# Kernel optimization log

Measured on AMD Instinct MI355X. Metric: run time of the kernel, lower is better.

The kernel has to match this reference:

```python
import jax, jax.numpy as jnp
import numpy as np

D_IN, D, N, L, NW, NC, NH, DC = 1536, 256, 16, 2, 64, 234, 4, 4
B_SZ, T_LEN = 256, 64
N_SITES, N_HOURS, META = 20, 24, 16


def setup_inputs() -> dict:
    key = jax.random.key(0)
    ks = iter(jax.random.split(key, 64))
    def rn(shape, scale=0.02):
        return jax.random.normal(next(ks), shape, jnp.float32) * scale
    inp = {}
    inp["emb"] = jax.random.normal(next(ks), (B_SZ, T_LEN, D_IN), jnp.float32)
    inp["perch_logits"] = jax.random.normal(next(ks), (B_SZ, T_LEN, NC), jnp.float32)
    inp["site_ids"] = jax.random.randint(next(ks), (B_SZ,), 0, N_SITES)
    inp["hours"] = jax.random.randint(next(ks), (B_SZ,), 0, N_HOURS)
    # input_proj: Linear(d_input, d_model) + LayerNorm
    inp["in_w"] = rn((D, D_IN)); inp["in_b"] = jnp.zeros((D,))
    inp["ln0_g"] = jnp.ones((D,)); inp["ln0_b"] = jnp.zeros((D,))
    inp["pos_enc"] = rn((1, NW, D))
    inp["site_emb"] = rn((N_SITES, META), 1.0)
    inp["hour_emb"] = rn((N_HOURS, META), 1.0)
    inp["meta_w"] = rn((D, 2 * META)); inp["meta_b"] = jnp.zeros((D,))
    # SelectiveSSM params, stacked [L, 2(dir)] over layers and fwd/bwd directions
    inp["ssm_in_w"] = rn((L, 2, 2 * D, D))
    inp["ssm_conv_w"] = rn((L, 2, D, DC), 0.1)
    inp["ssm_conv_b"] = jnp.zeros((L, 2, D))
    inp["ssm_dt_w"] = rn((L, 2, D, D)); inp["ssm_dt_b"] = jnp.zeros((L, 2, D))
    A = jnp.arange(1, N + 1, dtype=jnp.float32)
    inp["ssm_A_log"] = jnp.log(jnp.broadcast_to(A, (L, 2, D, N)))
    inp["ssm_Dp"] = jnp.ones((L, 2, D))
    inp["ssm_B_w"] = rn((L, 2, N, D)); inp["ssm_C_w"] = rn((L, 2, N, D))
    inp["merge_w"] = rn((L, D, 2 * D)); inp["merge_b"] = jnp.zeros((L, D))
    inp["ln_g"] = jnp.ones((L, D)); inp["ln_b"] = jnp.zeros((L, D))
    # TemporalCrossAttention
    inp["qkv_w"] = rn((3 * D, D)); inp["qkv_b"] = jnp.zeros((3 * D,))
    inp["ao_w"] = rn((D, D)); inp["ao_b"] = jnp.zeros((D,))
    inp["ca_ln1_g"] = jnp.ones((D,)); inp["ca_ln1_b"] = jnp.zeros((D,))
    inp["ffn_w1"] = rn((2 * D, D)); inp["ffn_b1"] = jnp.zeros((2 * D,))
    inp["ffn_w2"] = rn((D, 2 * D)); inp["ffn_b2"] = jnp.zeros((D,))
    inp["ca_ln2_g"] = jnp.ones((D,)); inp["ca_ln2_b"] = jnp.zeros((D,))
    # prototype head
    inp["prototypes"] = rn((NC, D))
    inp["proto_temp"] = jnp.asarray(5.0, jnp.float32)
    inp["class_bias"] = jnp.zeros((NC,))
    inp["fusion_alpha"] = jnp.zeros((NC,))
    return inp


def _ln(x, g, b, eps=1e-5):
    m = x.mean(-1, keepdims=True)
    v = ((x - m) ** 2).mean(-1, keepdims=True)
    return (x - m) * jax.lax.rsqrt(v + eps) * g + b


def _l2norm(x):
    n = jnp.sqrt((x * x).sum(-1, keepdims=True))
    return x / jnp.maximum(n, 1e-12)


def _ssm(x, in_w, conv_w, conv_b, dt_w, dt_b, A_log, Dp, B_w, C_w):
    """SelectiveSSM.forward. x: [B,T,D]. (z gate / out_proj unused in original.)"""
    Bb, T, Dd = x.shape
    x_ssm = (x @ in_w.T)[..., :Dd]  # first chunk of in_proj output
    # depthwise causal conv (Conv1d pad=DC-1 then slice [:T] == left pad)
    xp = jnp.pad(x_ssm, ((0, 0), (DC - 1, 0), (0, 0)))
    xc = sum(xp[:, k:k + T, :] * conv_w[:, k] for k in range(DC)) + conv_b
    xc = jax.nn.silu(xc)
    dt = jax.nn.softplus(xc @ dt_w.T + dt_b)       # [B,T,D]
    A = -jnp.exp(A_log)                            # [D,N]
    Bm = xc @ B_w.T                                # [B,T,N]
    Cm = xc @ C_w.T                                # [B,T,N]

    def step(h, inp):
        dt_t, B_t, C_t, x_t = inp                  # [B,D],[B,N],[B,N],[B,D]
        dA = jnp.exp(A * dt_t[..., None])          # [B,D,N]
        h = h * dA + (x_t * dt_t)[..., None] * B_t[:, None, :]
        y = jnp.einsum('bdn,bn->bd', h, C_t)
        return h, y

    h0 = jnp.zeros((Bb, Dd, A.shape[-1]), x.dtype)
    xs = (dt.transpose(1, 0, 2), Bm.transpose(1, 0, 2),
          Cm.transpose(1, 0, 2), x.transpose(1, 0, 2))
    _, ys = jax.lax.scan(step, h0, xs)             # ys: [T,B,D]
    return ys.transpose(1, 0, 2) + x * Dp


def _mha(x, qkv_w, qkv_b, ao_w, ao_b):
    Bb, T, Dd = x.shape
    dh = Dd // NH
    q, k, v = jnp.split(x @ qkv_w.T + qkv_b, 3, axis=-1)
    rs = lambda t: t.reshape(Bb, T, NH, dh).transpose(0, 2, 1, 3)
    q, k, v = rs(q), rs(k), rs(v)
    att = jax.nn.softmax(jnp.einsum('bhqd,bhkd->bhqk', q, k) / np.sqrt(dh), axis=-1)
    o = jnp.einsum('bhqk,bhkd->bhqd', att, v).transpose(0, 2, 1, 3).reshape(Bb, T, Dd)
    return o @ ao_w.T + ao_b


def reference(emb, perch_logits, site_ids, hours, in_w, in_b, ln0_g, ln0_b,
              pos_enc, site_emb, hour_emb, meta_w, meta_b,
              ssm_in_w, ssm_conv_w, ssm_conv_b, ssm_dt_w, ssm_dt_b,
              ssm_A_log, ssm_Dp, ssm_B_w, ssm_C_w, merge_w, merge_b, ln_g, ln_b,
              qkv_w, qkv_b, ao_w, ao_b, ca_ln1_g, ca_ln1_b,
              ffn_w1, ffn_b1, ffn_w2, ffn_b2, ca_ln2_g, ca_ln2_b,
              prototypes, proto_temp, class_bias, fusion_alpha):
    T = emb.shape[1]
    h = jax.nn.gelu(_ln(emb @ in_w.T + in_b, ln0_g, ln0_b), approximate=False)
    h = h + pos_enc[:, :T, :]
    meta = jnp.concatenate([site_emb[site_ids], hour_emb[hours]], -1) @ meta_w.T + meta_b
    h = h + meta[:, None, :]
    for l in range(L):
        res = h
        hf = _ssm(h, ssm_in_w[l, 0], ssm_conv_w[l, 0], ssm_conv_b[l, 0],
                  ssm_dt_w[l, 0], ssm_dt_b[l, 0], ssm_A_log[l, 0], ssm_Dp[l, 0],
                  ssm_B_w[l, 0], ssm_C_w[l, 0])
        hb = _ssm(h[:, ::-1], ssm_in_w[l, 1], ssm_conv_w[l, 1], ssm_conv_b[l, 1],
                  ssm_dt_w[l, 1], ssm_dt_b[l, 1], ssm_A_log[l, 1], ssm_Dp[l, 1],
                  ssm_B_w[l, 1], ssm_C_w[l, 1])[:, ::-1]
        h = jnp.concatenate([hf, hb], -1) @ merge_w[l].T + merge_b[l]
        h = _ln(h + res, ln_g[l], ln_b[l])
    # TemporalCrossAttention (pre-norm, residual)
    h = h + _mha(_ln(h, ca_ln1_g, ca_ln1_b), qkv_w, qkv_b, ao_w, ao_b)
    x2 = _ln(h, ca_ln2_g, ca_ln2_b)
    h = h + (jax.nn.gelu(x2 @ ffn_w1.T + ffn_b1, approximate=False) @ ffn_w2.T + ffn_b2)
    # prototype similarity head
    sim = (_l2norm(h) @ _l2norm(prototypes).T) * jax.nn.softplus(proto_temp) + class_bias
    alpha = jax.nn.sigmoid(fusion_alpha)
    species_logits = alpha * sim + (1.0 - alpha) * perch_logits
    return species_logits, h
```

## Files before the change

### kernel.cpp

```cpp
#include <hip/hip_runtime.h>
#include <math.h>

typedef float f32x4 __attribute__((ext_vector_type(4)));
typedef short bf16x8 __attribute__((ext_vector_type(8)));

#define DEV static __device__ __forceinline__

constexpr int MROWS = 16384;
constexpr long long MD = 4194304LL;
constexpr long long DTZ = 4718592LL;
constexpr float L2E = 1.44269504088896f;
constexpr float LN2 = 0.69314718055995f;

DEV short f2bf(float f) {
  unsigned u = __float_as_uint(f);
  u += 0x7fffu + ((u >> 16) & 1u);
  return (short)(u >> 16);
}
DEV float wredsum(float v) {
#pragma unroll
  for (int off = 32; off > 0; off >>= 1) v += __shfl_xor(v, off, 64);
  return v;
}
DEV float gelu_f(float x) { return 0.5f * x * (1.f + erff(x * 0.70710678118654752f)); }
DEV float softplus_fast(float x) {
  return (x > 20.f) ? x : log2f(1.f + exp2f(x * L2E)) * LN2;
}
DEV float sigmoid_fast(float x) { return 1.f / (1.f + exp2f(-x * L2E)); }

enum { E_NONE = 0, E_BIAS = 1, E_BIAS_RES = 2, E_GELU_BIAS = 3, E_SIM = 4, E_CONV = 5 };

template <int EPI>
__global__ __launch_bounds__(256) void gemm128(
    const float* __restrict__ A, const float* __restrict__ W, float* __restrict__ C,
    const float* __restrict__ bias, const float* __restrict__ res,
    int K, int ldc,
    long long az, long long wz, long long cz, long long bz,
    const float* __restrict__ xa, const float* __restrict__ xt) {
  constexpr int SBYTES = (EPI == E_CONV) ? 33280 : 27648;
  __shared__ __align__(16) char smem[SBYTES];
  short* As = (short*)smem;
  short* Bs = As + 128 * 72;
  const int z = blockIdx.z;
  A += (long long)z * az;
  W += (long long)z * wz;
  C += (long long)z * cz;
  const float* bi = bias ? bias + (long long)z * bz : bias;
  const int tid = threadIdx.x, lane = tid & 63, wid = tid >> 6;
  const int wm = wid >> 1, wn = wid & 1;
  const int rowBase = blockIdx.y * 128, colBase = blockIdx.x * 64;
  f32x4 acc[4][2];
#pragma unroll
  for (int m = 0; m < 4; ++m)
#pragma unroll
    for (int n = 0; n < 2; ++n) acc[m][n] = f32x4{0.f, 0.f, 0.f, 0.f};
  const int sr = tid >> 3, sc = (tid & 7) << 3;
  f32x4 ra[4][2], rb[2][2];

#define GLOAD(K0)                                                              \
  {                                                                            \
    _Pragma("unroll") for (int p = 0; p < 4; ++p) {                            \
      const float* sa = A + (long long)(rowBase + p * 32 + sr) * K + ((K0) + sc); \
      ra[p][0] = *(const f32x4*)sa;                                            \
      ra[p][1] = *(const f32x4*)(sa + 4);                                      \
    }                                                                          \
    _Pragma("unroll") for (int q = 0; q < 2; ++q) {                            \
      int wr = colBase + q * 32 + sr;                                          \
      wr = (wr < ldc) ? wr : (ldc - 1);                                        \
      const float* sb = W + (long long)wr * K + ((K0) + sc);                   \
      rb[q][0] = *(const f32x4*)sb;                                            \
      rb[q][1] = *(const f32x4*)(sb + 4);                                      \
    }                                                                          \
  }

  GLOAD(0);
  const int nsteps = K >> 6;
  for (int s = 0; s < nsteps; ++s) {
    __syncthreads();
#pragma unroll
    for (int p = 0; p < 4; ++p) {
      bf16x8 pa;
      pa[0] = f2bf(ra[p][0][0]); pa[1] = f2bf(ra[p][0][1]);
      pa[2] = f2bf(ra[p][0][2]); pa[3] = f2bf(ra[p][0][3]);
      pa[4] = f2bf(ra[p][1][0]); pa[5] = f2bf(ra[p][1][1]);
      pa[6] = f2bf(ra[p][1][2]); pa[7] = f2bf(ra[p][1][3]);
      *(bf16x8*)&As[(p * 32 + sr) * 72 + sc] = pa;
    }
#pragma unroll
    for (int q = 0; q < 2; ++q) {
      bf16x8 pb;
      pb[0] = f2bf(rb[q][0][0]); pb[1] = f2bf(rb[q][0][1]);
      pb[2] = f2bf(rb[q][0][2]); pb[3] = f2bf(rb[q][0][3]);
      pb[4] = f2bf(rb[q][1][0]); pb[5] = f2bf(rb[q][1][1]);
      pb[6] = f2bf(rb[q][1][2]); pb[7] = f2bf(rb[q][1][3]);
      *(bf16x8*)&Bs[(q * 32 + sr) * 72 + sc] = pb;
    }
    if (s + 1 < nsteps) GLOAD((s + 1) << 6);
    __syncthreads();
#pragma unroll
    for (int ks = 0; ks < 2; ++ks) {
      const int kb = ks * 32 + (lane >> 4) * 8;
      bf16x8 af[4], bw[2];
#pragma unroll
      for (int m = 0; m < 4; ++m)
        af[m] = *(const bf16x8*)&As[(wm * 64 + m * 16 + (lane & 15)) * 72 + kb];
#pragma unroll
      for (int n = 0; n < 2; ++n)
        bw[n] = *(const bf16x8*)&Bs[(wn * 32 + n * 16 + (lane & 15)) * 72 + kb];
#pragma unroll
      for (int m = 0; m < 4; ++m)
#pragma unroll
        for (int n = 0; n < 2; ++n)
          acc[m][n] = __builtin_amdgcn_mfma_f32_16x16x32_bf16(af[m], bw[n], acc[m][n], 0, 0, 0);
    }
  }
#undef GLOAD

  if constexpr (EPI == E_CONV) {
    float* SX = (float*)smem;
    __syncthreads();
#pragma unroll
    for (int m = 0; m < 4; ++m)
#pragma unroll
      for (int n = 0; n < 2; ++n)
#pragma unroll
        for (int r = 0; r < 4; ++r) {
          const int rl = wm * 64 + m * 16 + ((lane >> 4) << 2) + r;
          const int cl = wn * 32 + n * 16 + (lane & 15);
          SX[rl * 65 + cl] = acc[m][n][r];
        }
    __syncthreads();
    const int c = tid & 63, rg = tid >> 6;
    const int gcol = colBase + c;
    const float* cwp = xa + (long long)z * 1024 + gcol * 4;
    const float wv0 = cwp[0], wv1 = cwp[1], wv2 = cwp[2], wv3 = cwp[3];
    const float cbv = xt[z * 256 + gcol];
#pragma unroll 4
    for (int i = 0; i < 32; ++i) {
      const int lr = rg * 32 + i;
      const int seq = lr >> 6, tau = lr & 63;
      float a = cbv;
#pragma unroll
      for (int k = 0; k < 4; ++k) {
        const int sidx = tau - 3 + k;
        if (sidx >= 0) {
          const int srow = seq * 64 + (z ? 63 - sidx : sidx);
          const float wk = (k == 0) ? wv0 : (k == 1) ? wv1 : (k == 2) ? wv2 : wv3;
          a += SX[srow * 65 + c] * wk;
        }
      }
      a = a * sigmoid_fast(a);
      C[(long long)(rowBase + lr) * ldc + gcol] = a;
    }
    return;
  }

  float sps = 0.f;
  if (EPI == E_SIM) sps = softplus_fast(xt[0]);
#pragma unroll
  for (int m = 0; m < 4; ++m)
#pragma unroll
    for (int n = 0; n < 2; ++n)
#pragma unroll
      for (int r = 0; r < 4; ++r) {
        const int row = rowBase + wm * 64 + m * 16 + ((lane >> 4) << 2) + r;
        const int col = colBase + wn * 32 + n * 16 + (lane & 15);
        if (col < ldc) {
          float v = acc[m][n][r];
          if (EPI == E_BIAS || EPI == E_BIAS_RES || EPI == E_GELU_BIAS) v += bi[col];
          if (EPI == E_BIAS_RES) v += res[(long long)row * ldc + col];
          if (EPI == E_GELU_BIAS) v = gelu_f(v);
          if (EPI == E_SIM) {
            v = v * sps + bi[col];
            const float al = 1.f / (1.f + expf(-xa[col]));
            v = al * v + (1.f - al) * res[(long long)row * ldc + col];
          }
          C[(long long)row * ldc + col] = v;
        }
      }
}

__global__ __launch_bounds__(256) void prep_wcat(
    const float* __restrict__ dt_w, const float* __restrict__ dt_b,
    const float* __restrict__ Bw, const float* __restrict__ Cw,
    float* __restrict__ wcat, float* __restrict__ bcat) {
  const int r = blockIdx.x, ld = blockIdx.y, tid = threadIdx.x;
  float v;
  if (r < 256)      v = dt_w[(long long)ld * 65536 + r * 256 + tid];
  else if (r < 272) v = Bw[(long long)ld * 4096 + (r - 256) * 256 + tid];
  else              v = Cw[(long long)ld * 4096 + (r - 272) * 256 + tid];
  wcat[(long long)ld * 98304 + (long long)r * 256 + tid] = v;
  if (r == 0) bcat[ld * 288 + tid] = dt_b[ld * 256 + tid];
  if (r == 1 && tid < 32) bcat[ld * 288 + 256 + tid] = 0.f;
}

__global__ __launch_bounds__(256) void meta_kernel(
    const int* __restrict__ site_ids, const int* __restrict__ hours,
    const float* __restrict__ site_emb, const float* __restrict__ hour_emb,
    const float* __restrict__ meta_w, const float* __restrict__ meta_b,
    float* __restrict__ out) {
  const int b = blockIdx.x, d = threadIdx.x;
  const int si = site_ids[b], hr = hours[b];
  const float* mw = meta_w + d * 32;
  float acc = meta_b[d];
#pragma unroll
  for (int m = 0; m < 16; ++m) acc += site_emb[si * 16 + m] * mw[m];
#pragma unroll
  for (int m = 0; m < 16; ++m) acc += hour_emb[hr * 16 + m] * mw[16 + m];
  out[b * 256 + d] = acc;
}

template <int MODE>
__global__ __launch_bounds__(256) void ln_kernel(
    const float* __restrict__ in, float* __restrict__ out,
    const float* __restrict__ g, const float* __restrict__ bta,
    const float* __restrict__ pos, const float* __restrict__ mta) {
  const int row = blockIdx.x * 4 + (threadIdx.x >> 6);
  const int lane = threadIdx.x & 63;
  const long long base = (long long)row * 256 + lane * 4;
  f32x4 v = *(const f32x4*)(in + base);
  const float mean = wredsum(v[0] + v[1] + v[2] + v[3]) * (1.f / 256.f);
  f32x4 c = {v[0] - mean, v[1] - mean, v[2] - mean, v[3] - mean};
  const float var = wredsum(c[0] * c[0] + c[1] * c[1] + c[2] * c[2] + c[3] * c[3]) * (1.f / 256.f);
  const float rs = rsqrtf(var + 1e-5f);
  const f32x4 gv = *(const f32x4*)(g + lane * 4);
  const f32x4 bv = *(const f32x4*)(bta + lane * 4);
  f32x4 y;
#pragma unroll
  for (int j = 0; j < 4; ++j) y[j] = c[j] * rs * gv[j] + bv[j];
  if (MODE == 1) {
    const f32x4 pv = *(const f32x4*)(pos + (row & 63) * 256 + lane * 4);
    const f32x4 mv = *(const f32x4*)(mta + (row >> 6) * 256 + lane * 4);
#pragma unroll
    for (int j = 0; j < 4; ++j) y[j] = gelu_f(y[j]) + pv[j] + mv[j];
  }
  *(f32x4*)(out + base) = y;
}

__global__ __launch_bounds__(256) void scan_kernel(
    const float* __restrict__ dtbc, const float* __restrict__ x,
    float* __restrict__ hcat, const float* __restrict__ alog,
    const float* __restrict__ Dpl) {
  __shared__ float bcs[2048];
  const int b = blockIdx.x, dir = blockIdx.y, d = threadIdx.x;
  const float* dz = dtbc + (long long)dir * DTZ;
  for (int idx = d; idx < 2048; idx += 256)
    bcs[idx] = dz[(long long)(b * 64 + (idx >> 5)) * 288 + 256 + (idx & 31)];
  float an2[16];
  const float* al = alog + ((long long)dir * 256 + d) * 16;
#pragma unroll
  for (int n = 0; n < 16; ++n) an2[n] = -expf(al[n]) * L2E;
  const float dp = Dpl[dir * 256 + d];
  float hs[16];
#pragma unroll
  for (int n = 0; n < 16; ++n) hs[n] = 0.f;
  __syncthreads();
  const float* dtr = dz + (long long)b * 64 * 288 + d;
  const float* xr = x + (long long)b * 64 * 256 + d;
  float draw = dtr[0];
  float xv = xr[(dir ? 63 : 0) * 256];
  for (int tau = 0; tau < 64; ++tau) {
    float drawN = 0.f, xvN = 0.f;
    if (tau < 63) {
      drawN = dtr[(tau + 1) * 288];
      xvN = xr[(dir ? (62 - tau) : (tau + 1)) * 256];
    }
    const float dtv = softplus_fast(draw);
    const float u = xv * dtv;
    float y = 0.f;
#pragma unroll
    for (int n = 0; n < 16; ++n) {
      const float dA = exp2f(an2[n] * dtv);
      hs[n] = hs[n] * dA + u * bcs[tau * 32 + n];
      y += hs[n] * bcs[tau * 32 + 16 + n];
    }
    const int to = dir ? 63 - tau : tau;
    hcat[(long long)(b * 64 + to) * 512 + dir * 256 + d] = y + xv * dp;
    draw = drawN; xv = xvN;
  }
}

__global__ __launch_bounds__(64) void attn_kernel(
    const float* __restrict__ qkv, float* __restrict__ out) {
  __shared__ float ks[64 * 65], vs[64 * 65], ss[64 * 65];
  const int b = blockIdx.x, h = blockIdx.y, lane = threadIdx.x;
  const long long rb = (long long)b * 64;
  const float* base = qkv + rb * 768 + h * 64;
  for (int r = 0; r < 64; ++r) {
    ss[r * 65 + lane] = base[(long long)r * 768 + lane];
    ks[r * 65 + lane] = base[(long long)r * 768 + 256 + lane];
    vs[r * 65 + lane] = base[(long long)r * 768 + 512 + lane];
  }
  __syncthreads();
  float q[64];
#pragma unroll
  for (int e = 0; e < 64; ++e) q[e] = ss[lane * 65 + e];
  __syncthreads();
  float mx = -1e30f;
  for (int j = 0; j < 64; ++j) {
    float a = 0.f;
#pragma unroll
    for (int e = 0; e < 64; ++e) a += q[e] * ks[j * 65 + e];
    a *= 0.125f;
    ss[lane * 65 + j] = a;
    mx = fmaxf(mx, a);
  }
  float sum = 0.f;
  for (int j = 0; j < 64; ++j) {
    const float p = exp2f((ss[lane * 65 + j] - mx) * L2E);
    ss[lane * 65 + j] = p;
    sum += p;
  }
  const float inv = 1.f / sum;
  float o[64];
#pragma unroll
  for (int e = 0; e < 64; ++e) o[e] = 0.f;
  for (int j = 0; j < 64; ++j) {
    const float p = ss[lane * 65 + j] * inv;
#pragma unroll
    for (int e = 0; e < 64; ++e) o[e] += p * vs[j * 65 + e];
  }
  __syncthreads();
#pragma unroll
  for (int e = 0; e < 64; ++e) ss[lane * 65 + e] = o[e];
  __syncthreads();
  for (int r = 0; r < 64; ++r)
    out[(rb + r) * 256 + h * 64 + lane] = ss[r * 65 + lane];
}

__global__ __launch_bounds__(256) void hn_kernel(
    const float* __restrict__ in, float* __restrict__ hn, float* __restrict__ out1) {
  const int row = blockIdx.x * 4 + (threadIdx.x >> 6);
  const int lane = threadIdx.x & 63;
  const long long base = (long long)row * 256 + lane * 4;
  f32x4 v = *(const f32x4*)(in + base);
  const float ss = wredsum(v[0] * v[0] + v[1] * v[1] + v[2] * v[2] + v[3] * v[3]);
  const float inv = 1.f / fmaxf(sqrtf(ss), 1e-12f);
  f32x4 y = {v[0] * inv, v[1] * inv, v[2] * inv, v[3] * inv};
  *(f32x4*)(hn + base) = y;
  *(f32x4*)(out1 + base) = v;
}

__global__ __launch_bounds__(256) void protonorm_kernel(
    const float* __restrict__ proto, float* __restrict__ pn) {
  __shared__ float red[4];
  const int c = blockIdx.x, d = threadIdx.x;
  const float v = (c < 234) ? proto[(long long)c * 256 + d] : 0.f;
  float s = wredsum(v * v);
  if ((d & 63) == 0) red[d >> 6] = s;
  __syncthreads();
  const float ss = red[0] + red[1] + red[2] + red[3];
  const float inv = (c < 234) ? 1.f / fmaxf(sqrtf(ss), 1e-12f) : 0.f;
  pn[(long long)c * 256 + d] = v * inv;
}

extern "C" void kernel_launch(void* const* d_in, const int* in_sizes, int n_in,
                              void* d_out, int out_size, void* d_ws, size_t ws_size,
                              hipStream_t stream) {
  const float* emb       = (const float*)d_in[0];
  const float* perch     = (const float*)d_in[1];
  const int*   site_ids  = (const int*)d_in[2];
  const int*   hours     = (const int*)d_in[3];
  const float* in_w      = (const float*)d_in[4];
  const float* in_b      = (const float*)d_in[5];
  const float* ln0_g     = (const float*)d_in[6];
  const float* ln0_b     = (const float*)d_in[7];
  const float* pos_enc   = (const float*)d_in[8];
  const float* site_emb  = (const float*)d_in[9];
  const float* hour_emb  = (const float*)d_in[10];
  const float* meta_w    = (const float*)d_in[11];
  const float* meta_b    = (const float*)d_in[12];
  const float* ssm_in_w  = (const float*)d_in[13];
  const float* ssm_cw    = (const float*)d_in[14];
  const float* ssm_cb    = (const float*)d_in[15];
  const float* ssm_dt_w  = (const float*)d_in[16];
  const float* ssm_dt_b  = (const float*)d_in[17];
  const float* ssm_Alog  = (const float*)d_in[18];
  const float* ssm_Dp    = (const float*)d_in[19];
  const float* ssm_B_w   = (const float*)d_in[20];
  const float* ssm_C_w   = (const float*)d_in[21];
  const float* merge_w   = (const float*)d_in[22];
  const float* merge_b   = (const float*)d_in[23];
  const float* ln_g      = (const float*)d_in[24];
  const float* ln_b      = (const float*)d_in[25];
  const float* qkv_w     = (const float*)d_in[26];
  const float* qkv_b     = (const float*)d_in[27];
  const float* ao_w      = (const float*)d_in[28];
  const float* ao_b      = (const float*)d_in[29];
  const float* ca1_g     = (const float*)d_in[30];
  const float* ca1_b     = (const float*)d_in[31];
  const float* ffn_w1    = (const float*)d_in[32];
  const float* ffn_b1    = (const float*)d_in[33];
  const float* ffn_w2    = (const float*)d_in[34];
  const float* ffn_b2    = (const float*)d_in[35];
  const float* ca2_g     = (const float*)d_in[36];
  const float* ca2_b     = (const float*)d_in[37];
  const float* protos    = (const float*)d_in[38];
  const float* ptemp     = (const float*)d_in[39];
  const float* cbias     = (const float*)d_in[40];
  const float* falpha    = (const float*)d_in[41];

  float* out0 = (float*)d_out;
  float* out1 = out0 + (long long)MROWS * 234;

  float* ws = (float*)d_ws;
  float* w_meta = ws;
  float* w_h    = ws + 65536;
  float* w_tpre = w_h + MD;
  float* w_ar   = w_tpre + MD;
  float* w_xc   = w_ar;
  float* w_dtbc = w_ar + 2 * MD;
  float* w_wcat = w_ar + 2 * MD + 2 * DTZ;
  float* w_bcat = w_wcat + 393216;
  float* w_z    = w_ar;
  float* w_qkv  = w_ar + MD;
  float* w_mid  = w_ar + MD;
  float* w_hn   = w_ar;
  float* w_pn   = w_ar + MD;

  const dim3 blk(256);

  prep_wcat<<<dim3(288, 4), blk, 0, stream>>>(ssm_dt_w, ssm_dt_b, ssm_B_w,
                                              ssm_C_w, w_wcat, w_bcat);
  meta_kernel<<<256, blk, 0, stream>>>(site_ids, hours, site_emb, hour_emb,
                                       meta_w, meta_b, w_meta);
  gemm128<E_BIAS><<<dim3(4, 128, 1), blk, 0, stream>>>(
      emb, in_w, w_tpre, in_b, nullptr, 1536, 256, 0, 0, 0, 0, nullptr, nullptr);
  ln_kernel<1><<<MROWS / 4, blk, 0, stream>>>(w_tpre, w_h, ln0_g, ln0_b, pos_enc, w_meta);

  for (int l = 0; l < 2; ++l) {
    const float* inw_l = ssm_in_w + (long long)l * 262144;
    const float* cw_l  = ssm_cw + l * 2048;
    const float* cb_l  = ssm_cb + l * 512;
    const float* Al_l  = ssm_Alog + l * 8192;
    const float* Dp_l  = ssm_Dp + l * 512;

    gemm128<E_CONV><<<dim3(4, 128, 2), blk, 0, stream>>>(
        w_h, inw_l, w_xc, nullptr, nullptr, 256, 256,
        0LL, 131072LL, MD, 0LL, cw_l, cb_l);
    gemm128<E_BIAS><<<dim3(5, 128, 2), blk, 0, stream>>>(
        w_xc, w_wcat + (long long)l * 196608, w_dtbc,
        w_bcat + l * 576, nullptr, 256, 288,
        MD, 98304LL, DTZ, 288LL, nullptr, nullptr);
    scan_kernel<<<dim3(256, 2), blk, 0, stream>>>(w_dtbc, w_h, w_xc, Al_l, Dp_l);
    gemm128<E_BIAS_RES><<<dim3(4, 128, 1), blk, 0, stream>>>(
        w_xc, merge_w + (long long)l * 131072, w_tpre, merge_b + l * 256, w_h,
        512, 256, 0, 0, 0, 0, nullptr, nullptr);
    ln_kernel<0><<<MROWS / 4, blk, 0, stream>>>(w_tpre, w_h, ln_g + l * 256, ln_b + l * 256,
                                                nullptr, nullptr);
  }

  ln_kernel<0><<<MROWS / 4, blk, 0, stream>>>(w_h, w_z, ca1_g, ca1_b, nullptr, nullptr);
  gemm128<E_BIAS><<<dim3(12, 128, 1), blk, 0, stream>>>(
      w_z, qkv_w, w_qkv, qkv_b, nullptr, 256, 768, 0, 0, 0, 0, nullptr, nullptr);
  attn_kernel<<<dim3(256, 4), dim3(64), 0, stream>>>(w_qkv, w_tpre);
  gemm128<E_BIAS_RES><<<dim3(4, 128, 1), blk, 0, stream>>>(
      w_tpre, ao_w, w_h, ao_b, w_h, 256, 256, 0, 0, 0, 0, nullptr, nullptr);

  ln_kernel<0><<<MROWS / 4, blk, 0, stream>>>(w_h, w_z, ca2_g, ca2_b, nullptr, nullptr);
  gemm128<E_GELU_BIAS><<<dim3(8, 128, 1), blk, 0, stream>>>(
      w_z, ffn_w1, w_mid, ffn_b1, nullptr, 256, 512, 0, 0, 0, 0, nullptr, nullptr);
  gemm128<E_BIAS_RES><<<dim3(4, 128, 1), blk, 0, stream>>>(
      w_mid, ffn_w2, w_h, ffn_b2, w_h, 512, 256, 0, 0, 0, 0, nullptr, nullptr);

  protonorm_kernel<<<256, blk, 0, stream>>>(protos, w_pn);
  hn_kernel<<<MROWS / 4, blk, 0, stream>>>(w_h, w_hn, out1);
  gemm128<E_SIM><<<dim3(4, 128, 1), blk, 0, stream>>>(
      w_hn, w_pn, out0, cbias, perch, 256, 234, 0, 0, 0, 0, falpha, ptemp);

  (void)in_sizes; (void)n_in; (void)out_size; (void)ws_size;
}
```

Baseline: 825.6 us.

## Rewrite attention kernel with bf16 MFMA for QK^T and PV

Replaces the scalar fp32 per-lane attention, which computed QK^T and PV with 64x64 FMA loops out of LDS, with bf16 MFMA 16x16x32 instructions. Q, K and a transposed V are staged in LDS as bf16 using vectorized loads. Softmax runs on the accumulator fragments with cross-lane shuffles, and P is repacked by shuffles into the B operand layout. Output goes out through a padded LDS tile with vectorized stores. Rounding Q, K, V and P to bf16 lowers precision.

```diff
diff --git a/kernel.cpp b/kernel.cpp
--- a/kernel.cpp
+++ b/kernel.cpp
@@ -3,6 +3,7 @@
 
 typedef float f32x4 __attribute__((ext_vector_type(4)));
 typedef short bf16x8 __attribute__((ext_vector_type(8)));
+typedef unsigned u32x4 __attribute__((ext_vector_type(4)));
 
 #define DEV static __device__ __forceinline__
 
@@ -282,50 +283,144 @@
 
 __global__ __launch_bounds__(64) void attn_kernel(
     const float* __restrict__ qkv, float* __restrict__ out) {
-  __shared__ float ks[64 * 65], vs[64 * 65], ss[64 * 65];
+  __shared__ __align__(16) char smem[3 * 64 * 72 * 2];
+  short* qs  = (short*)smem;
+  short* kss = qs + 64 * 72;
+  short* vts = kss + 64 * 72;
   const int b = blockIdx.x, h = blockIdx.y, lane = threadIdx.x;
   const long long rb = (long long)b * 64;
   const float* base = qkv + rb * 768 + h * 64;
-  for (int r = 0; r < 64; ++r) {
-    ss[r * 65 + lane] = base[(long long)r * 768 + lane];
-    ks[r * 65 + lane] = base[(long long)r * 768 + 256 + lane];
-    vs[r * 65 + lane] = base[(long long)r * 768 + 512 + lane];
+  const int t3 = lane >> 3, oct = lane & 7;
+#pragma unroll
+  for (int p = 0; p < 8; ++p) {
+    const int r = p * 8 + t3;
+    const float* qp = base + (long long)r * 768 + oct * 8;
+    f32x4 a0 = *(const f32x4*)qp, a1 = *(const f32x4*)(qp + 4);
+    bf16x8 pa;
+    pa[0] = f2bf(a0[0]); pa[1] = f2bf(a0[1]); pa[2] = f2bf(a0[2]); pa[3] = f2bf(a0[3]);
+    pa[4] = f2bf(a1[0]); pa[5] = f2bf(a1[1]); pa[6] = f2bf(a1[2]); pa[7] = f2bf(a1[3]);
+    *(bf16x8*)&qs[r * 72 + oct * 8] = pa;
+    const float* kp = qp + 256;
+    f32x4 b0 = *(const f32x4*)kp, b1 = *(const f32x4*)(kp + 4);
+    bf16x8 pb;
+    pb[0] = f2bf(b0[0]); pb[1] = f2bf(b0[1]); pb[2] = f2bf(b0[2]); pb[3] = f2bf(b0[3]);
+    pb[4] = f2bf(b1[0]); pb[5] = f2bf(b1[1]); pb[6] = f2bf(b1[2]); pb[7] = f2bf(b1[3]);
+    *(bf16x8*)&kss[r * 72 + oct * 8] = pb;
+  }
+  {
+    f32x4 vr[16];
+#pragma unroll
+    for (int c = 0; c < 16; ++c)
+      vr[c] = *(const f32x4*)(base + (long long)lane * 768 + 512 + c * 4);
+#pragma unroll
+    for (int ee = 0; ee < 64; ++ee)
+      vts[ee * 72 + lane] = f2bf(vr[ee >> 2][ee & 3]);
   }
   __syncthreads();
-  float q[64];
-#pragma unroll
-  for (int e = 0; e < 64; ++e) q[e] = ss[lane * 65 + e];
+  const int g = lane >> 4, i16 = lane & 15;
+  f32x4 acc_s[4][4];
+#pragma unroll
+  for (int jt = 0; jt < 4; ++jt)
+#pragma unroll
+    for (int it = 0; it < 4; ++it) acc_s[jt][it] = f32x4{0.f, 0.f, 0.f, 0.f};
+#pragma unroll
+  for (int ks2 = 0; ks2 < 2; ++ks2) {
+    const int e0 = ks2 * 32 + g * 8;
+    bf16x8 af[4], bq[4];
+#pragma unroll
+    for (int jt = 0; jt < 4; ++jt)
+      af[jt] = *(const bf16x8*)&kss[(jt * 16 + i16) * 72 + e0];
+#pragma unroll
+    for (int it = 0; it < 4; ++it)
+      bq[it] = *(const bf16x8*)&qs[(it * 16 + i16) * 72 + e0];
+#pragma unroll
+    for (int jt = 0; jt < 4; ++jt)
+#pragma unroll
+      for (int it = 0; it < 4; ++it)
+        acc_s[jt][it] = __builtin_amdgcn_mfma_f32_16x16x32_bf16(af[jt], bq[it], acc_s[jt][it], 0, 0, 0);
+  }
+  float inv[4];
+  unsigned pu[4][4][2];
+#pragma unroll
+  for (int it = 0; it < 4; ++it) {
+    float m = -1e30f;
+#pragma unroll
+    for (int jt = 0; jt < 4; ++jt)
+#pragma unroll
+      for (int r = 0; r < 4; ++r) {
+        acc_s[jt][it][r] *= 0.125f;
+        m = fmaxf(m, acc_s[jt][it][r]);
+      }
+    m = fmaxf(m, __shfl_xor(m, 16, 64));
+    m = fmaxf(m, __shfl_xor(m, 32, 64));
+    float sum = 0.f;
+#pragma unroll
+    for (int jt = 0; jt < 4; ++jt)
+#pragma unroll
+      for (int r = 0; r < 4; ++r) {
+        const float pv = exp2f((acc_s[jt][it][r] - m) * L2E);
+        acc_s[jt][it][r] = pv;
+        sum += pv;
+      }
+    sum += __shfl_xor(sum, 16, 64);
+    sum += __shfl_xor(sum, 32, 64);
+    inv[it] = 1.f / sum;
+#pragma unroll
+    for (int jt = 0; jt < 4; ++jt) {
+      pu[jt][it][0] = ((unsigned)(unsigned short)f2bf(acc_s[jt][it][1]) << 16) |
+                      (unsigned)(unsigned short)f2bf(acc_s[jt][it][0]);
+      pu[jt][it][1] = ((unsigned)(unsigned short)f2bf(acc_s[jt][it][3]) << 16) |
+                      (unsigned)(unsigned short)f2bf(acc_s[jt][it][2]);
+    }
+  }
+  f32x4 acc_o[4][4];
+#pragma unroll
+  for (int mt = 0; mt < 4; ++mt)
+#pragma unroll
+    for (int it = 0; it < 4; ++it) acc_o[mt][it] = f32x4{0.f, 0.f, 0.f, 0.f};
+  const int srcA = ((lane >> 4) & 1) * 32 + i16;
+  const int srcB = srcA + 16;
+  const bool hi = (lane & 32) != 0;
+#pragma unroll
+  for (int ks2 = 0; ks2 < 2; ++ks2) {
+    const int j0 = ks2 * 32 + g * 8;
+    bf16x8 av[4];
+#pragma unroll
+    for (int mt = 0; mt < 4; ++mt)
+      av[mt] = *(const bf16x8*)&vts[(mt * 16 + i16) * 72 + j0];
+#pragma unroll
+    for (int it = 0; it < 4; ++it) {
+      unsigned w[4];
+#pragma unroll
+      for (int wd = 0; wd < 2; ++wd) {
+        const unsigned loA = (unsigned)__shfl((int)pu[2 * ks2 + 0][it][wd], srcA, 64);
+        const unsigned hiA = (unsigned)__shfl((int)pu[2 * ks2 + 1][it][wd], srcA, 64);
+        w[wd] = hi ? hiA : loA;
+        const unsigned loB = (unsigned)__shfl((int)pu[2 * ks2 + 0][it][wd], srcB, 64);
+        const unsigned hiB = (unsigned)__shfl((int)pu[2 * ks2 + 1][it][wd], srcB, 64);
+        w[2 + wd] = hi ? hiB : loB;
+      }
+      const u32x4 bb = {w[0], w[1], w[2], w[3]};
+      const bf16x8 pb = __builtin_bit_cast(bf16x8, bb);
+#pragma unroll
+      for (int mt = 0; mt < 4; ++mt)
+        acc_o[mt][it] = __builtin_amdgcn_mfma_f32_16x16x32_bf16(av[mt], pb, acc_o[mt][it], 0, 0, 0);
+    }
+  }
   __syncthreads();
-  float mx = -1e30f;
-  for (int j = 0; j < 64; ++j) {
-    float a = 0.f;
-#pragma unroll
-    for (int e = 0; e < 64; ++e) a += q[e] * ks[j * 65 + e];
-    a *= 0.125f;
-    ss[lane * 65 + j] = a;
-    mx = fmaxf(mx, a);
-  }
-  float sum = 0.f;
-  for (int j = 0; j < 64; ++j) {
-    const float p = exp2f((ss[lane * 65 + j] - mx) * L2E);
-    ss[lane * 65 + j] = p;
-    sum += p;
-  }
-  const float inv = 1.f / sum;
-  float o[64];
-#pragma unroll
-  for (int e = 0; e < 64; ++e) o[e] = 0.f;
-  for (int j = 0; j < 64; ++j) {
-    const float p = ss[lane * 65 + j] * inv;
-#pragma unroll
-    for (int e = 0; e < 64; ++e) o[e] += p * vs[j * 65 + e];
-  }
+  float* ot = (float*)smem;
+#pragma unroll
+  for (int mt = 0; mt < 4; ++mt)
+#pragma unroll
+    for (int it = 0; it < 4; ++it)
+#pragma unroll
+      for (int r = 0; r < 4; ++r)
+        ot[(it * 16 + i16) * 68 + mt * 16 + g * 4 + r] = acc_o[mt][it][r] * inv[it];
   __syncthreads();
-#pragma unroll
-  for (int e = 0; e < 64; ++e) ss[lane * 65 + e] = o[e];
-  __syncthreads();
-  for (int r = 0; r < 64; ++r)
-    out[(rb + r) * 256 + h * 64 + lane] = ss[r * 65 + lane];
+  float* orow = out + (rb + lane) * 256 + h * 64;
+#pragma unroll
+  for (int c = 0; c < 16; ++c)
+    *(f32x4*)(orow + c * 4) = *(const f32x4*)&ot[lane * 68 + c * 4];
 }
 
 __global__ __launch_bounds__(256) void hn_kernel(
```

Measured after the change: 770.5 us. 1.07x faster.
